# Optimization experiments

Measured on AMD Instinct MI355X. Metric: run time of the kernel, lower is better.

The kernel has to match this reference:

```python
import jax, jax.numpy as jnp
import numpy as np

C = jnp.complex64

def _ry_mat(t):
    c = jnp.cos(t / 2).astype(C)
    s = jnp.sin(t / 2).astype(C)
    return jnp.stack([jnp.stack([c, -s], -1), jnp.stack([s, c], -1)], -2)

def _rx_mat(t):
    c = jnp.cos(t / 2).astype(C)
    s = (-1j) * jnp.sin(t / 2).astype(C)
    return jnp.stack([jnp.stack([c, s], -1), jnp.stack([s, c], -1)], -2)

def _rz_mat(t):
    em = jnp.exp(-1j * (t / 2).astype(C))
    ep = jnp.exp(1j * (t / 2).astype(C))
    z = jnp.zeros_like(em)
    return jnp.stack([jnp.stack([em, z], -1), jnp.stack([z, ep], -1)], -2)

def _apply_1q(psi, gate, w):
    # psi: [bsz, 2^n]; gate: [2,2] (shared) or [bsz,2,2] (per-sample)
    bsz = psi.shape[0]
    s = psi.reshape(bsz, 1 << w, 2, -1)  # wire w isolated on axis 2
    if gate.ndim == 2:
        out = jnp.einsum('ij,bljr->blir', gate, s)
    else:
        out = jnp.einsum('bij,bljr->blir', gate, s)
    return out.reshape(bsz, -1)

def _apply_cnot(psi, c, t):
    bsz = psi.shape[0]
    a, b = min(c, t), max(c, t)
    s = psi.reshape(bsz, 1 << a, 2, 1 << (b - a - 1), 2, -1)
    if c < t:
        # control on axis 2, target on axis 4; after slicing ctrl=1, target -> axis 3
        s = s.at[:, :, 1].set(jnp.flip(s[:, :, 1], axis=3))
    else:
        # control on axis 4, target on axis 2
        s = s.at[:, :, :, :, 1].set(jnp.flip(s[:, :, :, :, 1], axis=2))
    return s.reshape(bsz, -1)

def setup_inputs() -> dict:
    key = jax.random.key(0)
    k1, k2 = jax.random.split(key)
    bsz, n_wires, n_qlayers = 1024, 14, 4
    x_raw = jax.random.normal(k1, (bsz, n_wires), dtype=jnp.float32)
    angles = jax.random.normal(k2, (n_qlayers, n_wires, 3), dtype=jnp.float32) * 0.1
    return {"x_raw": x_raw, "angles": angles}

def reference(x_raw, angles):
    L, n, _ = angles.shape
    bsz = x_raw.shape[0]
    x_enc = jnp.tanh(x_raw[:, :n]) * jnp.pi  # [bsz, n]
    # |0...0> statevector, wire 0 is the most significant bit
    psi = jnp.zeros((bsz, 1 << n), dtype=C).at[:, 0].set(1.0)
    # RY encoding (per-sample angles)
    for w in range(n):
        psi = _apply_1q(psi, _ry_mat(x_enc[:, w]), w)
    # variational layers
    for k in range(L):
        for w in range(n):
            psi = _apply_1q(psi, _rx_mat(angles[k, w, 0]), w)
            psi = _apply_1q(psi, _ry_mat(angles[k, w, 1]), w)
            psi = _apply_1q(psi, _rz_mat(angles[k, w, 2]), w)
        for i in range(n - 1):
            psi = _apply_cnot(psi, i, i + 1)
        psi = _apply_cnot(psi, n - 1, 0)
    # <Z_0>: +|amp|^2 when bit0=0, -|amp|^2 when bit0=1
    p = jnp.abs(psi.reshape(bsz, 2, -1)) ** 2
    return (p[:, 0].sum(-1) - p[:, 1].sum(-1)).astype(jnp.float32)
```

## Files before the change

### kernel.cpp

```cpp
#include <hip/hip_runtime.h>
#include <cmath>
#include <cstdint>

#define NW      14
#define NST     (1 << NW)
#define THREADS 512
#define NPASS   12
#define WTP     512

typedef _Float16 f16;
typedef _Float16 f16x8 __attribute__((ext_vector_type(8)));
typedef float    f32x4 __attribute__((ext_vector_type(4)));
typedef unsigned short u16;

struct PassArg { u16 Mm[4]; u16 Mt[3]; u16 Mw[3]; };
struct Plan { PassArg ps[NPASS]; u16 initM[14]; u16 measR; u16 _pad; };

__device__ __forceinline__ float2 cmulf(float2 a, float2 b) {
    return make_float2(a.x * b.x - a.y * b.y, a.x * b.y + a.y * b.x);
}
__device__ __forceinline__ unsigned swzu(unsigned s) {
    return s ^ ((((s >> 6) ^ (s >> 9) ^ (s >> 11)) & 7u) << 3);
}
__device__ __forceinline__ unsigned wtofs(unsigned m, unsigned q01) {
    return (m * 16 + q01 * 8) ^ (((m >> 2) & 1u) << 3);
}

__global__ __launch_bounds__(THREADS, 4)
void vqc_kernel(const float* __restrict__ x_raw, const float* __restrict__ angles,
                float* __restrict__ out, Plan pl)
{
    extern __shared__ char smem[];
    f16*    Sh  = (f16*)smem;
    f16*    Wt  = Sh + 2 * NST;
    float2* G   = (float2*)(Wt + NPASS * WTP);
    float*  red = (float*)G;

    const int b   = blockIdx.x;
    const int tid = threadIdx.x;
    const int lane = tid & 63, wv = tid >> 6;
    const int q = lane >> 4, m = lane & 15;

    if (tid < 4 * NW) {
        const int k = tid / NW, w = tid % NW;
        const float a  = angles[(k * NW + w) * 3 + 0];
        const float bb = angles[(k * NW + w) * 3 + 1];
        const float c  = angles[(k * NW + w) * 3 + 2];
        float sa, ca, sb, cb, sc, cc;
        sincosf(a * 0.5f, &sa, &ca);
        sincosf(bb * 0.5f, &sb, &cb);
        sincosf(c * 0.5f, &sc, &cc);
        float2 m00 = make_float2(cb * ca,  sb * sa);
        float2 m01 = make_float2(-sb * ca, -cb * sa);
        float2 m10 = make_float2(sb * ca,  -cb * sa);
        float2 m11 = make_float2(cb * ca,  -sb * sa);
        const float2 e0 = make_float2(cc, -sc), e1 = make_float2(cc, sc);
        float2 u00 = cmulf(e0, m00), u01 = cmulf(e0, m01);
        float2 u10 = cmulf(e1, m10), u11 = cmulf(e1, m11);
        if (k == 0) {
            const float xe = tanhf(x_raw[b * NW + w]) * 3.14159265358979f;
            float se, ce;
            sincosf(xe * 0.5f, &se, &ce);
            float2 v00 = make_float2(u00.x * ce + u01.x * se, u00.y * ce + u01.y * se);
            float2 v01 = make_float2(-u00.x * se + u01.x * ce, -u00.y * se + u01.y * ce);
            float2 v10 = make_float2(u10.x * ce + u11.x * se, u10.y * ce + u11.y * se);
            float2 v11 = make_float2(-u10.x * se + u11.x * ce, -u10.y * se + u11.y * ce);
            u00 = v00; u01 = v01; u10 = v10; u11 = v11;
        }
        const int gi = (k * NW + w) * 4;
        G[gi + 0] = u00; G[gi + 1] = u01; G[gi + 2] = u10; G[gi + 3] = u11;
    }
    __syncthreads();

    #pragma unroll
    for (int it = 0; it < 2; ++it) {
        const int t2 = tid + it * THREADS;
        if (t2 < NPASS * 64) {
            const int p = t2 >> 6, l6 = t2 & 63;
            const int ap = l6 & 15, ahalf = (l6 >> 4) & 1, dup = l6 >> 5;
            const int layer = (p >> 2) + 1, g = p & 3;

            float2 p3;
            if (g == 3) {
                p3 = make_float2((((ap >> 3) & 1) == ahalf) ? 1.f : 0.f, 0.f);
            } else {
                const int wire = 13 - (10 - 4 * g + 3);
                p3 = G[(layer * NW + wire) * 4 + ((ap >> 3) & 1) * 2 + ahalf];
            }
            float2 e0a, e0b, e1a, e1b, e2a, e2b;
            {
                const int r0 = ap & 1, r1 = (ap >> 1) & 1, r2 = (ap >> 2) & 1;
                if (g == 3) {
                    const float2* G13 = G + (layer * NW + 13) * 4;
                    const float2* G12 = G + (layer * NW + 12) * 4;
                    e0a = G13[r0 * 2 + 0]; e0b = G13[r0 * 2 + 1];
                    e1a = G12[r1 * 2 + 0]; e1b = G12[r1 * 2 + 1];
                    e2a = make_float2(r2 == 0 ? 1.f : 0.f, 0.f);
                    e2b = make_float2(r2 == 1 ? 1.f : 0.f, 0.f);
                } else {
                    const float2* G0 = G + (layer * NW + (13 - (10 - 4 * g + 0))) * 4;
                    const float2* G1 = G + (layer * NW + (13 - (10 - 4 * g + 1))) * 4;
                    const float2* G2 = G + (layer * NW + (13 - (10 - 4 * g + 2))) * 4;
                    e0a = G0[r0 * 2 + 0]; e0b = G0[r0 * 2 + 1];
                    e1a = G1[r1 * 2 + 0]; e1b = G1[r1 * 2 + 1];
                    e2a = G2[r2 * 2 + 0]; e2b = G2[r2 * 2 + 1];
                }
            }
            f16x8 frag;
            #pragma unroll
            for (int j2 = 0; j2 < 8; ++j2) {
                float2 v = cmulf(p3, (j2 & 4) ? e2b : e2a);
                v = cmulf(v, (j2 & 2) ? e1b : e1a);
                v = cmulf(v, (j2 & 1) ? e0b : e0a);
                frag[j2] = (f16)(dup ? v.y : v.x);
            }
            *(f16x8*)(Wt + p * WTP + dup * 256 + wtofs(ap, ahalf)) = frag;
        }
    }

    {
        float2 common = make_float2(1.f, 0.f);
        #pragma unroll
        for (int bit = 0; bit < 9; ++bit) {
            const int w = 13 - bit;
            const float2 f = ((tid >> bit) & 1) ? G[w * 4 + 2] : G[w * 4 + 0];
            common = cmulf(common, f);
        }
        unsigned p9 = 0;
        #pragma unroll
        for (int bit = 0; bit < 9; ++bit)
            p9 ^= ((tid >> bit) & 1) ? (unsigned)pl.initM[bit] : 0u;
        float2 f0[2], f1[2], f2[2], f3[2], f4[2];
        f0[0] = G[4*4+0]; f0[1] = G[4*4+2];
        f1[0] = G[3*4+0]; f1[1] = G[3*4+2];
        f2[0] = G[2*4+0]; f2[1] = G[2*4+2];
        f3[0] = G[1*4+0]; f3[1] = G[1*4+2];
        f4[0] = G[0*4+0]; f4[1] = G[0*4+2];
        #pragma unroll
        for (int j = 0; j < 32; ++j) {
            float2 o = cmulf(cmulf(f0[j & 1], f1[(j >> 1) & 1]),
                             cmulf(f2[(j >> 2) & 1], f3[(j >> 3) & 1]));
            o = cmulf(o, f4[(j >> 4) & 1]);
            const float2 amp = cmulf(common, o);
            const unsigned sj = ((j & 1) ? pl.initM[9] : 0) ^ ((j & 2) ? pl.initM[10] : 0)
                              ^ ((j & 4) ? pl.initM[11] : 0) ^ ((j & 8) ? pl.initM[12] : 0)
                              ^ ((j & 16) ? pl.initM[13] : 0);
            const unsigned ph = swzu(p9 ^ sj);
            Sh[ph]       = (f16)amp.x;
            Sh[ph + NST] = (f16)amp.y;
        }
    }
    __syncthreads();

    const unsigned plane_off = (unsigned)(q >> 1) << 14;
    const unsigned q01 = (unsigned)(q & 1);
    const f32x4 z4 = {0.f, 0.f, 0.f, 0.f};
    #pragma unroll
    for (int p = 0; p < NPASS; ++p) {
        const PassArg& P = pl.ps[p];
        const unsigned pm = ((m & 1) ? P.Mm[0] : 0) ^ ((m & 2) ? P.Mm[1] : 0)
                          ^ ((m & 4) ? P.Mm[2] : 0) ^ ((m & 8) ? P.Mm[3] : 0);
        const unsigned wb = ((wv & 1) ? P.Mw[0] : 0) ^ ((wv & 2) ? P.Mw[1] : 0)
                          ^ ((wv & 4) ? P.Mw[2] : 0);
        const unsigned b0 = pm ^ wb;
        const f16x8 tr = *(const f16x8*)(Wt + p * WTP +       wtofs((unsigned)m, q01));
        const f16x8 ti = *(const f16x8*)(Wt + p * WTP + 256 + wtofs((unsigned)m, q01));
        const f16x8 bf1 = (q < 2) ? tr : -ti;
        const f16x8 bf2 = (q < 2) ? ti : tr;
        unsigned sw[8];
        f16x8 av[8];
        #pragma unroll
        for (int tt = 0; tt < 8; ++tt) {
            const unsigned s0 = b0 ^ ((tt & 1) ? P.Mt[0] : 0)
                                   ^ ((tt & 2) ? P.Mt[1] : 0)
                                   ^ ((tt & 4) ? P.Mt[2] : 0);
            sw[tt] = swzu(s0);
            av[tt] = *(const f16x8*)(Sh + plane_off + (sw[tt] ^ (q01 << 3)));
        }
        __syncthreads();
        #pragma unroll
        for (int tt = 0; tt < 8; ++tt) {
            const f32x4 d1 = __builtin_amdgcn_mfma_f32_16x16x32_f16(av[tt], bf1, z4, 0, 0, 0);
            const f32x4 d2 = __builtin_amdgcn_mfma_f32_16x16x32_f16(av[tt], bf2, z4, 0, 0, 0);
            union { f16 h[4]; uint2 u; } c1, c2;
            #pragma unroll
            for (int r = 0; r < 4; ++r) { c1.h[r] = (f16)d1[r]; c2.h[r] = (f16)d2[r]; }
            const unsigned wu = sw[tt] ^ ((unsigned)q << 2);
            *(uint2*)(Sh + wu)       = c1.u;
            *(uint2*)(Sh + NST + wu) = c2.u;
        }
        __syncthreads();
    }

    float acc = 0.f;
    {
        const unsigned base = (unsigned)tid * 32;
        const unsigned swb  = swzu(base);
        const int pb = __popc(base & (unsigned)pl.measR) & 1;
        #pragma unroll
        for (int cch = 0; cch < 4; ++cch) {
            const unsigned co = (unsigned)cch * 8;
            const f16x8 rr = *(const f16x8*)(Sh + (swb ^ co));
            const f16x8 ii = *(const f16x8*)(Sh + NST + (swb ^ co));
            #pragma unroll
            for (int e = 0; e < 8; ++e) {
                const float re = (float)rr[e], im = (float)ii[e];
                const float pw = fmaf(re, re, im * im);
                const int sgn = pb ^ (__popc((co | (unsigned)e) & (unsigned)pl.measR) & 1);
                acc += sgn ? -pw : pw;
            }
        }
    }
    #pragma unroll
    for (int off = 32; off > 0; off >>= 1) acc += __shfl_down(acc, off);
    if ((tid & 63) == 0) red[wv] = acc;
    __syncthreads();
    if (tid == 0) {
        float s = 0.f;
        #pragma unroll
        for (int i = 0; i < THREADS / 64; ++i) s += red[i];
        out[b] = s;
    }
}

struct GFm { u16 col[14]; };

static unsigned ringp_host(unsigned x) {
    unsigned s = x;
    s ^= s >> 1; s ^= s >> 2; s ^= s >> 4; s ^= s >> 8;
    s &= 0x3FFFu;
    return (s ^ ((s & 1u) << 13)) & 0x3FFFu;
}
static u16 gf_apply(const GFm& m, u16 v) {
    u16 r = 0;
    for (int b = 0; b < 14; ++b) if ((v >> b) & 1) r ^= m.col[b];
    return r;
}
static GFm gf_compose(const GFm& A, const GFm& B) {
    GFm C;
    for (int b = 0; b < 14; ++b) C.col[b] = gf_apply(A, B.col[b]);
    return C;
}
static void rows_from(const GFm& A, u16 r[14]) {
    for (int i = 0; i < 14; ++i) {
        u16 mm = 0;
        for (int b = 0; b < 14; ++b) mm |= (u16)(((A.col[b] >> i) & 1) << b);
        r[i] = mm;
    }
}
static GFm from_rows(const u16 r[14]) {
    GFm A;
    for (int b = 0; b < 14; ++b) {
        u16 c = 0;
        for (int i = 0; i < 14; ++i) c |= (u16)(((r[i] >> b) & 1) << i);
        A.col[b] = c;
    }
    return A;
}
static GFm gf_inv(const GFm& A) {
    u16 M[14], I[14];
    rows_from(A, M);
    for (int i = 0; i < 14; ++i) I[i] = (u16)(1u << i);
    for (int c = 0; c < 14; ++c) {
        int p = c;
        while (p < 14 && !((M[p] >> c) & 1)) ++p;
        if (p == 14) continue;
        u16 t = M[c]; M[c] = M[p]; M[p] = t;
        t = I[c]; I[c] = I[p]; I[p] = t;
        for (int r2 = 0; r2 < 14; ++r2)
            if (r2 != c && ((M[r2] >> c) & 1)) { M[r2] ^= M[c]; I[r2] ^= I[c]; }
    }
    return from_rows(I);
}

static void build_plan(Plan& pl) {
    GFm ring, ringInv;
    for (int b = 0; b < 14; ++b) ring.col[b] = (u16)ringp_host(1u << b);
    ringInv = gf_inv(ring);

    GFm phi;
    for (int j = 0; j < 4; ++j) phi.col[10 + j] = (u16)(1u << j);
    for (int j = 0; j < 4; ++j) phi.col[6 + j]  = (u16)(1u << (4 + j));
    for (int j = 0; j < 4; ++j) phi.col[2 + j]  = (u16)(1u << (8 + j));
    phi.col[0] = (u16)(1u << 12);
    phi.col[1] = (u16)(1u << 13);

    for (int b = 0; b < 14; ++b) pl.initM[b] = gf_apply(phi, ring.col[b]);

    const int gb[4][4] = {{10,11,12,13},{6,7,8,9},{2,3,4,5},{0,1,6,7}};

    for (int p = 0; p < NPASS; ++p) {
        const int g = p & 3;
        u16 uv[4];
        if (g < 3) for (int j = 0; j < 4; ++j) uv[j] = (u16)(1u << gb[g + 1][j]);
        else       for (int j = 0; j < 4; ++j) uv[j] = ringInv.col[10 + j];
        for (int j = 0; j < 4; ++j) pl.ps[p].Mm[j] = gf_apply(phi, uv[j]);

        u16 span[14]; int ns = 0;
        u16 tv[6]; int nt = 0;
        auto tryAdd = [&](u16 v) -> bool {
            bool ch = true;
            while (ch) {
                ch = false;
                for (int i = 0; i < ns; ++i) {
                    const int tb = 31 - __builtin_clz((unsigned)span[i]);
                    if ((v >> tb) & 1) { v ^= span[i]; ch = true; }
                }
            }
            if (!v) return false;
            span[ns++] = v;
            return true;
        };
        for (int j = 0; j < 4; ++j) tryAdd((u16)(1u << gb[g][j]));
        for (int j = 0; j < 4; ++j) tryAdd(uv[j]);
        for (int b2 = 0; b2 < 14 && nt < 6; ++b2)
            if (tryAdd((u16)(1u << b2))) tv[nt++] = (u16)(1u << b2);
        for (int i = 0; i < 3; ++i) pl.ps[p].Mt[i] = gf_apply(phi, tv[i]);
        for (int i = 0; i < 3; ++i) pl.ps[p].Mw[i] = gf_apply(phi, tv[i + 3]);

        GFm Bm;
        for (int j = 0; j < 4; ++j) Bm.col[j]     = (u16)(1u << gb[g][j]);
        for (int j = 0; j < 4; ++j) Bm.col[4 + j] = uv[j];
        for (int i = 0; i < 6; ++i) Bm.col[8 + i] = tv[i];
        GFm Binv = gf_inv(Bm);
        u16 img[14];
        for (int j = 0; j < 4; ++j) img[j]     = pl.ps[p].Mm[j];
        for (int j = 0; j < 4; ++j) img[4 + j] = (u16)(1u << j);
        for (int i = 0; i < 6; ++i) img[8 + i] = gf_apply(phi, tv[i]);
        GFm nphi;
        for (int b2 = 0; b2 < 14; ++b2) {
            const u16 coef = gf_apply(Binv, (u16)(1u << b2));
            u16 v = 0;
            for (int j = 0; j < 14; ++j) if ((coef >> j) & 1) v ^= img[j];
            nphi.col[b2] = v;
        }
        if (g == 3) nphi = gf_compose(nphi, ringInv);
        phi = nphi;
    }

    GFm pinv = gf_inv(phi);
    u16 rows[14];
    rows_from(pinv, rows);
    pl.measR = rows[13];
    pl._pad = 0;
}

extern "C" void kernel_launch(void* const* d_in, const int* in_sizes, int n_in,
                              void* d_out, int out_size, void* d_ws, size_t ws_size,
                              hipStream_t stream) {
    const float* x_raw  = (const float*)d_in[0];
    const float* angles = (const float*)d_in[1];
    float* out = (float*)d_out;
    const int bsz = in_sizes[0] / NW;

    Plan pl;
    build_plan(pl);

    const size_t lds = (size_t)2 * NST * sizeof(f16)
                     + (size_t)NPASS * WTP * sizeof(f16)
                     + (size_t)4 * NW * 4 * sizeof(float2);
    (void)hipFuncSetAttribute((const void*)vqc_kernel,
                              hipFuncAttributeMaxDynamicSharedMemorySize, (int)lds);
    vqc_kernel<<<dim3(bsz), dim3(THREADS), lds, stream>>>(x_raw, angles, out, pl);
}
```

Before: 118.9 us.

## Hoist batch-invariant gate weight construction into pre-kernel and fold swizzle into plan masks

The per-block construction of the shared-angle gate weight fragments and layer-0 variational matrices moves into a single-block pre-kernel that writes them to workspace. Each main block now copies those fragments into LDS and only computes its per-sample encoding columns. The LDS swizzle function is linear over GF(2), so it is folded on the host into the XOR masks of the plan, and the measurement parity mask gets the transposed version. This removes the per-address swizzle arithmetic. The cost is an extra kernel launch, a global-memory read per block, and a dependency between the two kernels.

After: 111.9 us. 5.9% less time.

```diff
diff --git a/kernel.cpp b/kernel.cpp
--- a/kernel.cpp
+++ b/kernel.cpp
@@ -2,11 +2,12 @@
 #include <cmath>
 #include <cstdint>
 
-#define NW      14
-#define NST     (1 << NW)
-#define THREADS 512
-#define NPASS   12
-#define WTP     512
+#define NW       14
+#define NST      (1 << NW)
+#define THREADS  512
+#define PRETHR   768
+#define NPASS    12
+#define WTP      512
 
 typedef _Float16 f16;
 typedef _Float16 f16x8 __attribute__((ext_vector_type(8)));
@@ -19,27 +20,16 @@
 __device__ __forceinline__ float2 cmulf(float2 a, float2 b) {
     return make_float2(a.x * b.x - a.y * b.y, a.x * b.y + a.y * b.x);
 }
-__device__ __forceinline__ unsigned swzu(unsigned s) {
-    return s ^ ((((s >> 6) ^ (s >> 9) ^ (s >> 11)) & 7u) << 3);
-}
-__device__ __forceinline__ unsigned wtofs(unsigned m, unsigned q01) {
+__device__ __host__ __forceinline__ unsigned wtofs(unsigned m, unsigned q01) {
     return (m * 16 + q01 * 8) ^ (((m >> 2) & 1u) << 3);
 }
 
-__global__ __launch_bounds__(THREADS, 4)
-void vqc_kernel(const float* __restrict__ x_raw, const float* __restrict__ angles,
-                float* __restrict__ out, Plan pl)
+__global__ __launch_bounds__(PRETHR)
+void vqc_pre(const float* __restrict__ angles, f16* __restrict__ wt_g,
+             float2* __restrict__ u0_g)
 {
-    extern __shared__ char smem[];
-    f16*    Sh  = (f16*)smem;
-    f16*    Wt  = Sh + 2 * NST;
-    float2* G   = (float2*)(Wt + NPASS * WTP);
-    float*  red = (float*)G;
-
-    const int b   = blockIdx.x;
+    __shared__ float2 G[4 * NW * 4];
     const int tid = threadIdx.x;
-    const int lane = tid & 63, wv = tid >> 6;
-    const int q = lane >> 4, m = lane & 15;
 
     if (tid < 4 * NW) {
         const int k = tid / NW, w = tid % NW;
@@ -55,75 +45,98 @@
         float2 m10 = make_float2(sb * ca,  -cb * sa);
         float2 m11 = make_float2(cb * ca,  -sb * sa);
         const float2 e0 = make_float2(cc, -sc), e1 = make_float2(cc, sc);
-        float2 u00 = cmulf(e0, m00), u01 = cmulf(e0, m01);
-        float2 u10 = cmulf(e1, m10), u11 = cmulf(e1, m11);
-        if (k == 0) {
-            const float xe = tanhf(x_raw[b * NW + w]) * 3.14159265358979f;
-            float se, ce;
-            sincosf(xe * 0.5f, &se, &ce);
-            float2 v00 = make_float2(u00.x * ce + u01.x * se, u00.y * ce + u01.y * se);
-            float2 v01 = make_float2(-u00.x * se + u01.x * ce, -u00.y * se + u01.y * ce);
-            float2 v10 = make_float2(u10.x * ce + u11.x * se, u10.y * ce + u11.y * se);
-            float2 v11 = make_float2(-u10.x * se + u11.x * ce, -u10.y * se + u11.y * ce);
-            u00 = v00; u01 = v01; u10 = v10; u11 = v11;
-        }
+        const float2 u00 = cmulf(e0, m00), u01 = cmulf(e0, m01);
+        const float2 u10 = cmulf(e1, m10), u11 = cmulf(e1, m11);
         const int gi = (k * NW + w) * 4;
         G[gi + 0] = u00; G[gi + 1] = u01; G[gi + 2] = u10; G[gi + 3] = u11;
+        if (k == 0) {
+            u0_g[w * 4 + 0] = u00; u0_g[w * 4 + 1] = u01;
+            u0_g[w * 4 + 2] = u10; u0_g[w * 4 + 3] = u11;
+        }
     }
     __syncthreads();
 
-    #pragma unroll
-    for (int it = 0; it < 2; ++it) {
-        const int t2 = tid + it * THREADS;
-        if (t2 < NPASS * 64) {
-            const int p = t2 >> 6, l6 = t2 & 63;
-            const int ap = l6 & 15, ahalf = (l6 >> 4) & 1, dup = l6 >> 5;
-            const int layer = (p >> 2) + 1, g = p & 3;
-
-            float2 p3;
+    {
+        const int p = tid >> 6, l6 = tid & 63;
+        const int ap = l6 & 15, ahalf = (l6 >> 4) & 1, dup = l6 >> 5;
+        const int layer = (p >> 2) + 1, g = p & 3;
+
+        float2 p3;
+        if (g == 3) {
+            p3 = make_float2((((ap >> 3) & 1) == ahalf) ? 1.f : 0.f, 0.f);
+        } else {
+            const int wire = 13 - (10 - 4 * g + 3);
+            p3 = G[(layer * NW + wire) * 4 + ((ap >> 3) & 1) * 2 + ahalf];
+        }
+        float2 e0a, e0b, e1a, e1b, e2a, e2b;
+        {
+            const int r0 = ap & 1, r1 = (ap >> 1) & 1, r2 = (ap >> 2) & 1;
             if (g == 3) {
-                p3 = make_float2((((ap >> 3) & 1) == ahalf) ? 1.f : 0.f, 0.f);
+                const float2* G13 = G + (layer * NW + 13) * 4;
+                const float2* G12 = G + (layer * NW + 12) * 4;
+                e0a = G13[r0 * 2 + 0]; e0b = G13[r0 * 2 + 1];
+                e1a = G12[r1 * 2 + 0]; e1b = G12[r1 * 2 + 1];
+                e2a = make_float2(r2 == 0 ? 1.f : 0.f, 0.f);
+                e2b = make_float2(r2 == 1 ? 1.f : 0.f, 0.f);
             } else {
-                const int wire = 13 - (10 - 4 * g + 3);
-                p3 = G[(layer * NW + wire) * 4 + ((ap >> 3) & 1) * 2 + ahalf];
+                const float2* G0 = G + (layer * NW + (13 - (10 - 4 * g + 0))) * 4;
+                const float2* G1 = G + (layer * NW + (13 - (10 - 4 * g + 1))) * 4;
+                const float2* G2 = G + (layer * NW + (13 - (10 - 4 * g + 2))) * 4;
+                e0a = G0[r0 * 2 + 0]; e0b = G0[r0 * 2 + 1];
+                e1a = G1[r1 * 2 + 0]; e1b = G1[r1 * 2 + 1];
+                e2a = G2[r2 * 2 + 0]; e2b = G2[r2 * 2 + 1];
             }
-            float2 e0a, e0b, e1a, e1b, e2a, e2b;
-            {
-                const int r0 = ap & 1, r1 = (ap >> 1) & 1, r2 = (ap >> 2) & 1;
-                if (g == 3) {
-                    const float2* G13 = G + (layer * NW + 13) * 4;
-                    const float2* G12 = G + (layer * NW + 12) * 4;
-                    e0a = G13[r0 * 2 + 0]; e0b = G13[r0 * 2 + 1];
-                    e1a = G12[r1 * 2 + 0]; e1b = G12[r1 * 2 + 1];
-                    e2a = make_float2(r2 == 0 ? 1.f : 0.f, 0.f);
-                    e2b = make_float2(r2 == 1 ? 1.f : 0.f, 0.f);
-                } else {
-                    const float2* G0 = G + (layer * NW + (13 - (10 - 4 * g + 0))) * 4;
-                    const float2* G1 = G + (layer * NW + (13 - (10 - 4 * g + 1))) * 4;
-                    const float2* G2 = G + (layer * NW + (13 - (10 - 4 * g + 2))) * 4;
-                    e0a = G0[r0 * 2 + 0]; e0b = G0[r0 * 2 + 1];
-                    e1a = G1[r1 * 2 + 0]; e1b = G1[r1 * 2 + 1];
-                    e2a = G2[r2 * 2 + 0]; e2b = G2[r2 * 2 + 1];
-                }
-            }
-            f16x8 frag;
-            #pragma unroll
-            for (int j2 = 0; j2 < 8; ++j2) {
-                float2 v = cmulf(p3, (j2 & 4) ? e2b : e2a);
-                v = cmulf(v, (j2 & 2) ? e1b : e1a);
-                v = cmulf(v, (j2 & 1) ? e0b : e0a);
-                frag[j2] = (f16)(dup ? v.y : v.x);
-            }
-            *(f16x8*)(Wt + p * WTP + dup * 256 + wtofs(ap, ahalf)) = frag;
-        }
-    }
+        }
+        f16x8 frag;
+        #pragma unroll
+        for (int j2 = 0; j2 < 8; ++j2) {
+            float2 v = cmulf(p3, (j2 & 4) ? e2b : e2a);
+            v = cmulf(v, (j2 & 2) ? e1b : e1a);
+            v = cmulf(v, (j2 & 1) ? e0b : e0a);
+            frag[j2] = (f16)(dup ? v.y : v.x);
+        }
+        *(f16x8*)(wt_g + p * WTP + dup * 256 + wtofs(ap, ahalf)) = frag;
+    }
+}
+
+__global__ __launch_bounds__(THREADS, 4)
+void vqc_kernel(const float* __restrict__ x_raw, const f16* __restrict__ wt_g,
+                const float2* __restrict__ u0_g, float* __restrict__ out, Plan pl)
+{
+    extern __shared__ char smem[];
+    f16*    Sh  = (f16*)smem;
+    f16*    Wt  = Sh + 2 * NST;
+    float2* G0c = (float2*)(Wt + NPASS * WTP);
+    float*  red = (float*)(G0c + 2 * NW);
+
+    const int b   = blockIdx.x;
+    const int tid = threadIdx.x;
+    const int lane = tid & 63, wv = tid >> 6;
+    const int q = lane >> 4, m = lane & 15;
+
+    {
+        const uint4* src = (const uint4*)wt_g;
+        uint4* dst = (uint4*)Wt;
+        dst[tid] = src[tid];
+        if (tid < 256) dst[512 + tid] = src[512 + tid];
+    }
+    if (tid < NW) {
+        const float xe = tanhf(x_raw[b * NW + tid]) * 3.14159265358979f;
+        float se, ce;
+        sincosf(xe * 0.5f, &se, &ce);
+        const float2 u00 = u0_g[tid * 4 + 0], u01 = u0_g[tid * 4 + 1];
+        const float2 u10 = u0_g[tid * 4 + 2], u11 = u0_g[tid * 4 + 3];
+        G0c[tid * 2 + 0] = make_float2(u00.x * ce + u01.x * se, u00.y * ce + u01.y * se);
+        G0c[tid * 2 + 1] = make_float2(u10.x * ce + u11.x * se, u10.y * ce + u11.y * se);
+    }
+    __syncthreads();
 
     {
         float2 common = make_float2(1.f, 0.f);
         #pragma unroll
         for (int bit = 0; bit < 9; ++bit) {
             const int w = 13 - bit;
-            const float2 f = ((tid >> bit) & 1) ? G[w * 4 + 2] : G[w * 4 + 0];
+            const float2 f = ((tid >> bit) & 1) ? G0c[w * 2 + 1] : G0c[w * 2 + 0];
             common = cmulf(common, f);
         }
         unsigned p9 = 0;
@@ -131,21 +144,21 @@
         for (int bit = 0; bit < 9; ++bit)
             p9 ^= ((tid >> bit) & 1) ? (unsigned)pl.initM[bit] : 0u;
         float2 f0[2], f1[2], f2[2], f3[2], f4[2];
-        f0[0] = G[4*4+0]; f0[1] = G[4*4+2];
-        f1[0] = G[3*4+0]; f1[1] = G[3*4+2];
-        f2[0] = G[2*4+0]; f2[1] = G[2*4+2];
-        f3[0] = G[1*4+0]; f3[1] = G[1*4+2];
-        f4[0] = G[0*4+0]; f4[1] = G[0*4+2];
+        f0[0] = G0c[4*2+0]; f0[1] = G0c[4*2+1];
+        f1[0] = G0c[3*2+0]; f1[1] = G0c[3*2+1];
+        f2[0] = G0c[2*2+0]; f2[1] = G0c[2*2+1];
+        f3[0] = G0c[1*2+0]; f3[1] = G0c[1*2+1];
+        f4[0] = G0c[0*2+0]; f4[1] = G0c[0*2+1];
         #pragma unroll
         for (int j = 0; j < 32; ++j) {
             float2 o = cmulf(cmulf(f0[j & 1], f1[(j >> 1) & 1]),
                              cmulf(f2[(j >> 2) & 1], f3[(j >> 3) & 1]));
             o = cmulf(o, f4[(j >> 4) & 1]);
             const float2 amp = cmulf(common, o);
-            const unsigned sj = ((j & 1) ? pl.initM[9] : 0) ^ ((j & 2) ? pl.initM[10] : 0)
-                              ^ ((j & 4) ? pl.initM[11] : 0) ^ ((j & 8) ? pl.initM[12] : 0)
-                              ^ ((j & 16) ? pl.initM[13] : 0);
-            const unsigned ph = swzu(p9 ^ sj);
+            const unsigned ph = p9
+                ^ ((j & 1) ? pl.initM[9]  : 0) ^ ((j & 2)  ? pl.initM[10] : 0)
+                ^ ((j & 4) ? pl.initM[11] : 0) ^ ((j & 8)  ? pl.initM[12] : 0)
+                ^ ((j & 16) ? pl.initM[13] : 0);
             Sh[ph]       = (f16)amp.x;
             Sh[ph + NST] = (f16)amp.y;
         }
@@ -171,10 +184,9 @@
         f16x8 av[8];
         #pragma unroll
         for (int tt = 0; tt < 8; ++tt) {
-            const unsigned s0 = b0 ^ ((tt & 1) ? P.Mt[0] : 0)
-                                   ^ ((tt & 2) ? P.Mt[1] : 0)
-                                   ^ ((tt & 4) ? P.Mt[2] : 0);
-            sw[tt] = swzu(s0);
+            sw[tt] = b0 ^ ((tt & 1) ? P.Mt[0] : 0)
+                        ^ ((tt & 2) ? P.Mt[1] : 0)
+                        ^ ((tt & 4) ? P.Mt[2] : 0);
             av[tt] = *(const f16x8*)(Sh + plane_off + (sw[tt] ^ (q01 << 3)));
         }
         __syncthreads();
@@ -195,13 +207,12 @@
     float acc = 0.f;
     {
         const unsigned base = (unsigned)tid * 32;
-        const unsigned swb  = swzu(base);
         const int pb = __popc(base & (unsigned)pl.measR) & 1;
         #pragma unroll
         for (int cch = 0; cch < 4; ++cch) {
             const unsigned co = (unsigned)cch * 8;
-            const f16x8 rr = *(const f16x8*)(Sh + (swb ^ co));
-            const f16x8 ii = *(const f16x8*)(Sh + NST + (swb ^ co));
+            const f16x8 rr = *(const f16x8*)(Sh + (base ^ co));
+            const f16x8 ii = *(const f16x8*)(Sh + NST + (base ^ co));
             #pragma unroll
             for (int e = 0; e < 8; ++e) {
                 const float re = (float)rr[e], im = (float)ii[e];
@@ -345,6 +356,26 @@
     pl._pad = 0;
 }
 
+static u16 swz_h(u16 v) {
+    return (u16)(v ^ ((((v >> 6) ^ (v >> 9) ^ (v >> 11)) & 7u) << 3));
+}
+static u16 swzT_h(u16 r) {
+    u16 o = r;
+    if ((r >> 3) & 1) o ^= (u16)((1u << 6) | (1u << 9)  | (1u << 11));
+    if ((r >> 4) & 1) o ^= (u16)((1u << 7) | (1u << 10) | (1u << 12));
+    if ((r >> 5) & 1) o ^= (u16)((1u << 8) | (1u << 11) | (1u << 13));
+    return o;
+}
+static void fold_swzu(Plan& pl) {
+    for (int p = 0; p < NPASS; ++p) {
+        for (int j = 0; j < 4; ++j) pl.ps[p].Mm[j] = swz_h(pl.ps[p].Mm[j]);
+        for (int j = 0; j < 3; ++j) pl.ps[p].Mt[j] = swz_h(pl.ps[p].Mt[j]);
+        for (int j = 0; j < 3; ++j) pl.ps[p].Mw[j] = swz_h(pl.ps[p].Mw[j]);
+    }
+    for (int b = 0; b < 14; ++b) pl.initM[b] = swz_h(pl.initM[b]);
+    pl.measR = swzT_h(pl.measR);
+}
+
 extern "C" void kernel_launch(void* const* d_in, const int* in_sizes, int n_in,
                               void* d_out, int out_size, void* d_ws, size_t ws_size,
                               hipStream_t stream) {
@@ -355,11 +386,18 @@
 
     Plan pl;
     build_plan(pl);
+    fold_swzu(pl);
+
+    f16*    wt_g = (f16*)d_ws;
+    float2* u0_g = (float2*)((char*)d_ws + (size_t)NPASS * WTP * sizeof(f16));
+
+    vqc_pre<<<dim3(1), dim3(PRETHR), 0, stream>>>(angles, wt_g, u0_g);
 
     const size_t lds = (size_t)2 * NST * sizeof(f16)
                      + (size_t)NPASS * WTP * sizeof(f16)
-                     + (size_t)4 * NW * 4 * sizeof(float2);
+                     + (size_t)(2 * NW) * sizeof(float2)
+                     + (size_t)(THREADS / 64) * sizeof(float);
     (void)hipFuncSetAttribute((const void*)vqc_kernel,
                               hipFuncAttributeMaxDynamicSharedMemorySize, (int)lds);
-    vqc_kernel<<<dim3(bsz), dim3(THREADS), lds, stream>>>(x_raw, angles, out, pl);
-}
+    vqc_kernel<<<dim3(bsz), dim3(THREADS), lds, stream>>>(x_raw, wt_g, u0_g, out, pl);
+}
```
